# Kernel tuning notes

Measured on AMD Instinct MI355X. Metric: run time of the kernel, lower is better.

The kernel has to match this reference:

```python
import jax, jax.numpy as jnp
import numpy as np

B, H, S, D = 2, 8, 2048, 64
ALPHA = 1
P_NORM = 2
EPS = 1e-5


def setup_inputs() -> dict:
    key = jax.random.key(0)
    kq, kk, kv = jax.random.split(key, 3)
    query = jax.random.normal(kq, (B, H, S, D), dtype=jnp.float32)
    keys = jax.random.normal(kk, (B, H, S, D), dtype=jnp.float32)
    vals = jax.random.normal(kv, (B, H, S, D), dtype=jnp.float32)
    # causal mask: 1 where attention allowed, 0 elsewhere (masked_fill on mask==0)
    mask = jnp.tril(jnp.ones((S, S), dtype=jnp.int32))[None, None, :, :]
    return {"query": query, "keys": keys, "vals": vals, "mask": mask}


def reference(query, keys, vals, mask):
    d = query.shape[-1]
    sqrt_d = jnp.asarray(d, query.dtype) ** 0.5
    # L2-normalized cosine similarity term
    q_n = query / jnp.linalg.norm(query, axis=-1, keepdims=True)
    k_n = keys / jnp.linalg.norm(keys, axis=-1, keepdims=True)
    cos = jnp.einsum('bhqd,bhkd->bhqk', q_n, k_n)
    rq = (1.0 + (1.0 - cos) / (ALPHA * sqrt_d)) ** (-ALPHA)
    preattn = jnp.log(rq + EPS)
    # magnitude term: (||q||_p^p + ||k||_p^p) / (2 sqrt(d))
    q_mag = jnp.sum(jnp.abs(query) ** P_NORM, axis=-1, keepdims=True)  # [B,H,S,1]
    k_mag = jnp.sum(jnp.abs(keys) ** P_NORM, axis=-1, keepdims=True)   # [B,H,S,1]
    preattn = preattn + (q_mag + jnp.swapaxes(k_mag, -2, -1)) / (2.0 * sqrt_d)
    preattn = jnp.where(mask == 0, -jnp.inf, preattn)
    attn = jax.nn.softmax(preattn, axis=-1)
    out = jnp.einsum('bhqk,bhkd->bhqd', attn, vals)
    return out, attn
```

## Files before the change

kernel.cpp:

```cpp
#include <hip/hip_runtime.h>
#include <math.h>


#define BH 16
#define SS 2048
#define DD 64
#define NKT 32

typedef float f4a __attribute__((ext_vector_type(4)));
typedef short bs8 __attribute__((ext_vector_type(8)));
typedef short bs4 __attribute__((ext_vector_type(4)));

__device__ __forceinline__ short bf16rne(float f) {
  unsigned u = __float_as_uint(f);
  u += 0x7fffu + ((u >> 16) & 1u);
  return (short)(u >> 16);
}

__device__ __forceinline__ void bf16split(float f, short& hi, short& lo) {
  unsigned u = __float_as_uint(f);
  hi = (short)(u >> 16);
  float r = f - __uint_as_float(u & 0xffff0000u);
  lo = (short)(__float_as_uint(r) >> 16);
}

__global__ __launch_bounds__(256) void rq_rowss(const float* __restrict__ q,
                                                const float* __restrict__ k,
                                                float* __restrict__ ws) {
  int gid = blockIdx.x * 256 + threadIdx.x;
  int grp = gid >> 4;
  int lane = gid & 15;
  const int nrows = BH * SS;
  const float* src = (grp < nrows) ? q : k;
  int row = (grp < nrows) ? grp : (grp - nrows);
  float4 v = *(const float4*)(src + (size_t)row * DD + lane * 4);
  float s = v.x * v.x + v.y * v.y + v.z * v.z + v.w * v.w;
  s += __shfl_xor(s, 1);
  s += __shfl_xor(s, 2);
  s += __shfl_xor(s, 4);
  s += __shfl_xor(s, 8);
  if (lane == 0) ws[grp] = s;
}

__global__ __launch_bounds__(256) void rq_attn(const float* __restrict__ Q,
                                               const float* __restrict__ K,
                                               const float* __restrict__ V,
                                               const float* __restrict__ ss,
                                               float* __restrict__ outp,
                                               float* __restrict__ attnp) {
  __shared__ short Kf[4096];
  __shared__ short Vhi[4096];
  __shared__ short Vlo[4096];
  __shared__ float aLds[64 * 69];
  __shared__ float ektS[64];
  __shared__ float lrowp[2][64];
  __shared__ float lrow[64];

  const int t = threadIdx.x;
  const int bx = blockIdx.x;
  const int qt = NKT - 1 - (bx >> 4);
  const int bh = bx & 15;
  const int qbase = qt * 64;
  const float* Qg = Q + (size_t)bh * SS * DD;
  const float* Kg = K + (size_t)bh * SS * DD;
  const float* Vg = V + (size_t)bh * SS * DD;
  float* Ag = attnp + (size_t)bh * SS * SS;
  const float* qss = ss + (size_t)bh * SS;
  const float* kss = ss + (size_t)(BH * SS) + (size_t)bh * SS;

  const int l = t & 63;
  const int wv = t >> 6;
  const int qrh = wv >> 1;
  const int kch = wv & 1;
  const int l15 = l & 15;
  const int lh = (l >> 4) & 3;

  const int ukb = ((((l15 >> 2) & 3) | (((lh >> 1) & 1) << 2) | ((lh & 1) << 3) |
                    ((l15 & 3) << 4)) << 3);
  const int uvb = ((((l15 >> 2) & 3) | ((lh & 1) << 2) | ((l & 3) << 3) |
                    (((lh >> 1) & 1) << 7)) << 3);

  const int s_rb = (t >> 4) << 2;
  const int s_c0 = (t & 15) << 2;
  const int kw_ks = s_c0 >> 5;
  const int kw_dgrp = (s_c0 >> 3) & 3;
  const int kw_e0 = s_c0 & 7;
  const int kw_ub = (((t >> 4) & 3) | (((kw_dgrp >> 1) & 1) << 2) |
                     ((kw_dgrp & 1) << 3) | (((t >> 4) >> 2) << 6));
  const int vw_ks = s_rb >> 5;
  const int vw_kcgrp = (s_rb >> 3) & 3;
  const int vw_e0 = s_rb & 7;
  const int vw_ub = (((t & 15) & 3) | ((vw_kcgrp & 1) << 2) |
                     ((((t & 15) >> 2) & 3) << 5) | (((vw_kcgrp >> 1) & 1) << 7));

  auto stageK = [&](int kbase) {
#pragma unroll
    for (int i = 0; i < 4; ++i) {
      const int kc = s_rb + i;
      float4 v = *(const float4*)(Kg + (size_t)(kbase + kc) * DD + s_c0);
      float rn = rsqrtf(kss[kbase + kc]);
      bs4 b;
      b[0] = bf16rne(v.x * rn);
      b[1] = bf16rne(v.y * rn);
      b[2] = bf16rne(v.z * rn);
      b[3] = bf16rne(v.w * rn);
      *(bs4*)&Kf[kw_ks * 2048 + (kw_ub | (i << 4)) * 8 + kw_e0] = b;
    }
    if (t < 64) ektS[t] = __expf(kss[kbase + t] * 0.0625f);
  };

  bs8 qf[2][2];
#pragma unroll
  for (int mb = 0; mb < 2; ++mb) {
    const int row = qbase + qrh * 32 + mb * 16 + l15;
    const float rn = rsqrtf(qss[row]);
#pragma unroll
    for (int ks = 0; ks < 2; ++ks) {
      const float* src = Qg + (size_t)row * DD + ks * 32 + lh * 8;
      float4 x = *(const float4*)src;
      float4 y = *(const float4*)(src + 4);
      bs8 q;
      q[0] = bf16rne(x.x * rn);
      q[1] = bf16rne(x.y * rn);
      q[2] = bf16rne(x.z * rn);
      q[3] = bf16rne(x.w * rn);
      q[4] = bf16rne(y.x * rn);
      q[5] = bf16rne(y.y * rn);
      q[6] = bf16rne(y.z * rn);
      q[7] = bf16rne(y.w * rn);
      qf[mb][ks] = q;
    }
  }

  const f4a fz = {0.f, 0.f, 0.f, 0.f};

  float rs[8] = {0.f, 0.f, 0.f, 0.f, 0.f, 0.f, 0.f, 0.f};
  for (int kt = 0; kt <= qt; ++kt) {
    const int kbase = kt * 64;
    stageK(kbase);
    __syncthreads();

    f4a acc[4];
    acc[0] = fz; acc[1] = fz; acc[2] = fz; acc[3] = fz;
#pragma unroll
    for (int ks = 0; ks < 2; ++ks)
#pragma unroll
      for (int nb = 0; nb < 2; ++nb) {
        bs8 kf = *(const bs8*)&Kf[ks * 2048 + ((kch * 2 + nb) << 9) + ukb];
#pragma unroll
        for (int mb = 0; mb < 2; ++mb)
          acc[mb * 2 + nb] = __builtin_amdgcn_mfma_f32_16x16x32_bf16(
              qf[mb][ks], kf, acc[mb * 2 + nb], 0, 0, 0);
      }

    const float ek0 = ektS[kch * 32 + l15];
    const float ek1 = ektS[kch * 32 + 16 + l15];
    const bool diag = (kt == qt);
#pragma unroll
    for (int mb = 0; mb < 2; ++mb)
#pragma unroll
      for (int nb = 0; nb < 2; ++nb)
#pragma unroll
        for (int r = 0; r < 4; ++r) {
          float w = fmaf(8.0f, __builtin_amdgcn_rcpf(9.0f - acc[mb * 2 + nb][r]),
                         1e-5f) * (nb ? ek1 : ek0);
          const int col = kch * 32 + nb * 16 + l15;
          const int rowl = qrh * 32 + mb * 16 + lh * 4 + r;
          if (diag && col > rowl) w = 0.0f;
          rs[mb * 4 + r] += w;
        }
    __syncthreads();
  }

#pragma unroll
  for (int e = 0; e < 8; ++e) {
    float s = rs[e];
    s += __shfl_xor(s, 1);
    s += __shfl_xor(s, 2);
    s += __shfl_xor(s, 4);
    s += __shfl_xor(s, 8);
    rs[e] = s;
  }
  if (l15 == 0) {
#pragma unroll
    for (int mb = 0; mb < 2; ++mb)
#pragma unroll
      for (int r = 0; r < 4; ++r)
        lrowp[kch][qrh * 32 + mb * 16 + lh * 4 + r] = rs[mb * 4 + r];
  }
  __syncthreads();
  if (t < 64) lrow[t] = 1.0f / (lrowp[0][t] + lrowp[1][t]);
  __syncthreads();

  float li[8];
#pragma unroll
  for (int mb = 0; mb < 2; ++mb)
#pragma unroll
    for (int r = 0; r < 4; ++r)
      li[mb * 4 + r] = lrow[qrh * 32 + mb * 16 + lh * 4 + r];

  f4a O[4];
  O[0] = fz; O[1] = fz; O[2] = fz; O[3] = fz;
  for (int kt = 0; kt <= qt; ++kt) {
    const int kbase = kt * 64;
    stageK(kbase);
    {
      float mm[4][4];
#pragma unroll
      for (int i = 0; i < 4; ++i)
        *(float4*)&mm[i][0] =
            *(const float4*)(Vg + (size_t)(kbase + s_rb + i) * DD + s_c0);
#pragma unroll
      for (int j = 0; j < 4; ++j) {
        bs4 h4, l4;
#pragma unroll
        for (int i = 0; i < 4; ++i) {
          short hh, ll;
          bf16split(mm[i][j], hh, ll);
          h4[i] = hh;
          l4[i] = ll;
        }
        const int idx = vw_ks * 2048 + (vw_ub | (j << 3)) * 8 + vw_e0;
        *(bs4*)&Vhi[idx] = h4;
        *(bs4*)&Vlo[idx] = l4;
      }
    }
    __syncthreads();

    f4a acc[4];
    acc[0] = fz; acc[1] = fz; acc[2] = fz; acc[3] = fz;
#pragma unroll
    for (int ks = 0; ks < 2; ++ks)
#pragma unroll
      for (int nb = 0; nb < 2; ++nb) {
        bs8 kf = *(const bs8*)&Kf[ks * 2048 + ((kch * 2 + nb) << 9) + ukb];
#pragma unroll
        for (int mb = 0; mb < 2; ++mb)
          acc[mb * 2 + nb] = __builtin_amdgcn_mfma_f32_16x16x32_bf16(
              qf[mb][ks], kf, acc[mb * 2 + nb], 0, 0, 0);
      }

    {
      const float ek0 = ektS[kch * 32 + l15];
      const float ek1 = ektS[kch * 32 + 16 + l15];
      const bool diag = (kt == qt);
#pragma unroll
      for (int mb = 0; mb < 2; ++mb)
#pragma unroll
        for (int nb = 0; nb < 2; ++nb)
#pragma unroll
          for (int r = 0; r < 4; ++r) {
            float w = fmaf(8.0f,
                           __builtin_amdgcn_rcpf(9.0f - acc[mb * 2 + nb][r]),
                           1e-5f) * (nb ? ek1 : ek0);
            const int col = kch * 32 + nb * 16 + l15;
            const int rowl = qrh * 32 + mb * 16 + lh * 4 + r;
            if (diag && col > rowl) w = 0.0f;
            aLds[rowl * 69 + col] = w * li[mb * 4 + r];
          }
    }
    __syncthreads();

    {
      const int c0 = (t & 15) << 2;
      const int qr0 = t >> 4;
#pragma unroll
      for (int it = 0; it < 4; ++it) {
        const int qr = qr0 + it * 16;
        const float* ap = &aLds[qr * 69 + c0];
        *(float4*)(Ag + (size_t)(qbase + qr) * SS + kbase + c0) =
            make_float4(ap[0], ap[1], ap[2], ap[3]);
      }
    }

#pragma unroll
    for (int ks = 0; ks < 2; ++ks) {
      bs8 AH[2], AL[2];
#pragma unroll
      for (int mb = 0; mb < 2; ++mb) {
        const float* ap =
            &aLds[(qrh * 32 + mb * 16 + l15) * 69 + ks * 32 + lh * 8];
        bs8 hh, ll;
#pragma unroll
        for (int e = 0; e < 8; ++e) {
          short h, lo2;
          bf16split(ap[e], h, lo2);
          hh[e] = h;
          ll[e] = lo2;
        }
        AH[mb] = hh;
        AL[mb] = ll;
      }
#pragma unroll
      for (int nb = 0; nb < 2; ++nb) {
        const int vidx = ks * 2048 + ((kch * 2 + nb) << 8) + uvb;
        bs8 VH = *(const bs8*)&Vhi[vidx];
        bs8 VL = *(const bs8*)&Vlo[vidx];
#pragma unroll
        for (int mb = 0; mb < 2; ++mb) {
          O[mb * 2 + nb] = __builtin_amdgcn_mfma_f32_16x16x32_bf16(
              AH[mb], VH, O[mb * 2 + nb], 0, 0, 0);
          O[mb * 2 + nb] = __builtin_amdgcn_mfma_f32_16x16x32_bf16(
              AH[mb], VL, O[mb * 2 + nb], 0, 0, 0);
          O[mb * 2 + nb] = __builtin_amdgcn_mfma_f32_16x16x32_bf16(
              AL[mb], VH, O[mb * 2 + nb], 0, 0, 0);
        }
      }
    }
    __syncthreads();
  }

  {
    const float4 z = make_float4(0.f, 0.f, 0.f, 0.f);
    const int r0 = (t >> 4) << 2;
    const int c0 = (t & 15) << 2;
    for (int kt = qt + 1; kt < NKT; ++kt) {
#pragma unroll
      for (int i = 0; i < 4; ++i)
        *(float4*)(Ag + (size_t)(qbase + r0 + i) * SS + kt * 64 + c0) = z;
    }
  }

  {
    float* Og = outp + (size_t)bh * SS * DD;
#pragma unroll
    for (int mb = 0; mb < 2; ++mb)
#pragma unroll
      for (int nb = 0; nb < 2; ++nb)
#pragma unroll
        for (int r = 0; r < 4; ++r) {
          const int row = qbase + qrh * 32 + mb * 16 + lh * 4 + r;
          const int col = kch * 32 + nb * 16 + l15;
          Og[(size_t)row * DD + col] = O[mb * 2 + nb][r];
        }
  }
}

extern "C" void kernel_launch(void* const* d_in, const int* in_sizes, int n_in,
                              void* d_out, int out_size, void* d_ws, size_t ws_size,
                              hipStream_t stream) {
  const float* q = (const float*)d_in[0];
  const float* k = (const float*)d_in[1];
  const float* v = (const float*)d_in[2];
  float* out = (float*)d_out;
  float* attn = out + (size_t)BH * SS * DD;
  float* ws = (float*)d_ws;

  rq_rowss<<<dim3((2 * BH * SS) / 16), dim3(256), 0, stream>>>(q, k, ws);
  rq_attn<<<dim3(NKT * 16), dim3(256), 0, stream>>>(q, k, v, ws, out, attn);
}
```

Baseline: 386.6 us.

## Keep attention probabilities in registers by transposing QK^T MFMA and splitting PV over keys

Swaps the MFMA operands so the score accumulator comes out transposed, which lets each lane build the bf16 hi/lo A-fragments for the PV product directly in registers. This removes the aLds staging buffer and one barrier per tile. Attention-matrix writes become direct nontemporal float4 stores from registers, and V is stored transposed in an XOR-swizzled layout for 16x16x16 MFMAs. Each wave now accumulates over its half of the keys for all 64 dims, so a final LDS reduction across the two waves is needed. The row-sum reduction now uses fewer shuffles, and launch bounds request 3 blocks per CU.

```diff
diff --git a/kernel.cpp b/kernel.cpp
--- a/kernel.cpp
+++ b/kernel.cpp
@@ -10,18 +10,30 @@
 typedef float f4a __attribute__((ext_vector_type(4)));
 typedef short bs8 __attribute__((ext_vector_type(8)));
 typedef short bs4 __attribute__((ext_vector_type(4)));
+typedef unsigned int u32x2 __attribute__((ext_vector_type(2)));
 
 __device__ __forceinline__ short bf16rne(float f) {
   unsigned u = __float_as_uint(f);
   u += 0x7fffu + ((u >> 16) & 1u);
   return (short)(u >> 16);
 }
-
-__device__ __forceinline__ void bf16split(float f, short& hi, short& lo) {
-  unsigned u = __float_as_uint(f);
-  hi = (short)(u >> 16);
-  float r = f - __uint_as_float(u & 0xffff0000u);
-  lo = (short)(__float_as_uint(r) >> 16);
+__device__ __forceinline__ float truncb(float x) {
+  return __uint_as_float(__float_as_uint(x) & 0xffff0000u);
+}
+__device__ __forceinline__ unsigned packhi(float lo, float hi) {
+  return (__float_as_uint(hi) & 0xffff0000u) | (__float_as_uint(lo) >> 16);
+}
+
+__device__ __forceinline__ f4a mfma16(bs4 a, bs4 b, f4a c) {
+#if __has_builtin(__builtin_amdgcn_mfma_f32_16x16x16bf16_1k)
+  return __builtin_amdgcn_mfma_f32_16x16x16bf16_1k(a, b, c, 0, 0, 0);
+#else
+  f4a d;
+  asm("v_mfma_f32_16x16x16_bf16 %0, %1, %2, %3"
+      : "=v"(d)
+      : "v"(a), "v"(b), "v"(c));
+  return d;
+#endif
 }
 
 __global__ __launch_bounds__(256) void rq_rowss(const float* __restrict__ q,
@@ -42,19 +54,19 @@
   if (lane == 0) ws[grp] = s;
 }
 
-__global__ __launch_bounds__(256) void rq_attn(const float* __restrict__ Q,
-                                               const float* __restrict__ K,
-                                               const float* __restrict__ V,
-                                               const float* __restrict__ ss,
-                                               float* __restrict__ outp,
-                                               float* __restrict__ attnp) {
-  __shared__ short Kf[4096];
-  __shared__ short Vhi[4096];
-  __shared__ short Vlo[4096];
-  __shared__ float aLds[64 * 69];
+__global__ __launch_bounds__(256, 3) void rq_attn(const float* __restrict__ Q,
+                                                  const float* __restrict__ K,
+                                                  const float* __restrict__ V,
+                                                  const float* __restrict__ ss,
+                                                  float* __restrict__ outp,
+                                                  float* __restrict__ attnp) {
+  __shared__ short smemS[12288];
   __shared__ float ektS[64];
   __shared__ float lrowp[2][64];
   __shared__ float lrow[64];
+  short* const Kf = smemS;
+  short* const VtH = smemS + 4096;
+  short* const VtL = smemS + 8192;
 
   const int t = threadIdx.x;
   const int bx = blockIdx.x;
@@ -73,12 +85,10 @@
   const int qrh = wv >> 1;
   const int kch = wv & 1;
   const int l15 = l & 15;
-  const int lh = (l >> 4) & 3;
-
-  const int ukb = ((((l15 >> 2) & 3) | (((lh >> 1) & 1) << 2) | ((lh & 1) << 3) |
-                    ((l15 & 3) << 4)) << 3);
-  const int uvb = ((((l15 >> 2) & 3) | ((lh & 1) << 2) | ((l & 3) << 3) |
-                    (((lh >> 1) & 1) << 7)) << 3);
+  const int lh = l >> 4;
+
+  const int ukb = ((((l15 >> 2) & 3) | (((lh >> 1) & 1) << 2) |
+                    ((lh & 1) << 3) | ((l15 & 3) << 4)) << 3);
 
   const int s_rb = (t >> 4) << 2;
   const int s_c0 = (t & 15) << 2;
@@ -87,11 +97,6 @@
   const int kw_e0 = s_c0 & 7;
   const int kw_ub = (((t >> 4) & 3) | (((kw_dgrp >> 1) & 1) << 2) |
                      ((kw_dgrp & 1) << 3) | (((t >> 4) >> 2) << 6));
-  const int vw_ks = s_rb >> 5;
-  const int vw_kcgrp = (s_rb >> 3) & 3;
-  const int vw_e0 = s_rb & 7;
-  const int vw_ub = (((t & 15) & 3) | ((vw_kcgrp & 1) << 2) |
-                     ((((t & 15) >> 2) & 3) << 5) | (((vw_kcgrp >> 1) & 1) << 7));
 
   auto stageK = [&](int kbase) {
 #pragma unroll
@@ -107,6 +112,31 @@
       *(bs4*)&Kf[kw_ks * 2048 + (kw_ub | (i << 4)) * 8 + kw_e0] = b;
     }
     if (t < 64) ektS[t] = __expf(kss[kbase + t] * 0.0625f);
+  };
+
+  auto stageV = [&](int kbase) {
+    float mm[4][4];
+#pragma unroll
+    for (int i = 0; i < 4; ++i)
+      *(float4*)&mm[i][0] =
+          *(const float4*)(Vg + (size_t)(kbase + s_rb + i) * DD + s_c0);
+    const int kgw = t >> 4;
+#pragma unroll
+    for (int j = 0; j < 4; ++j) {
+      const int d = s_c0 + j;
+      const int si = (d * 16 + (kgw ^ (d & 15))) * 4;
+      u32x2 h, lo2;
+      h.x = packhi(mm[0][j], mm[1][j]);
+      h.y = packhi(mm[2][j], mm[3][j]);
+      float r0 = mm[0][j] - truncb(mm[0][j]);
+      float r1 = mm[1][j] - truncb(mm[1][j]);
+      float r2 = mm[2][j] - truncb(mm[2][j]);
+      float r3 = mm[3][j] - truncb(mm[3][j]);
+      lo2.x = packhi(r0, r1);
+      lo2.y = packhi(r2, r3);
+      *(u32x2*)&VtH[si] = h;
+      *(u32x2*)&VtL[si] = lo2;
+    }
   };
 
   bs8 qf[2][2];
@@ -134,7 +164,7 @@
 
   const f4a fz = {0.f, 0.f, 0.f, 0.f};
 
-  float rs[8] = {0.f, 0.f, 0.f, 0.f, 0.f, 0.f, 0.f, 0.f};
+  float rs0 = 0.f, rs1 = 0.f;
   for (int kt = 0; kt <= qt; ++kt) {
     const int kbase = kt * 64;
     stageK(kbase);
@@ -150,81 +180,55 @@
 #pragma unroll
         for (int mb = 0; mb < 2; ++mb)
           acc[mb * 2 + nb] = __builtin_amdgcn_mfma_f32_16x16x32_bf16(
-              qf[mb][ks], kf, acc[mb * 2 + nb], 0, 0, 0);
-      }
-
-    const float ek0 = ektS[kch * 32 + l15];
-    const float ek1 = ektS[kch * 32 + 16 + l15];
+              kf, qf[mb][ks], acc[mb * 2 + nb], 0, 0, 0);
+      }
+
     const bool diag = (kt == qt);
 #pragma unroll
-    for (int mb = 0; mb < 2; ++mb)
-#pragma unroll
-      for (int nb = 0; nb < 2; ++nb)
+    for (int nb = 0; nb < 2; ++nb) {
+      float ekr[4];
+#pragma unroll
+      for (int r = 0; r < 4; ++r)
+        ekr[r] = ektS[kch * 32 + nb * 16 + lh * 4 + r];
+#pragma unroll
+      for (int mb = 0; mb < 2; ++mb) {
+        const int qg = qrh * 32 + mb * 16 + l15;
 #pragma unroll
         for (int r = 0; r < 4; ++r) {
-          float w = fmaf(8.0f, __builtin_amdgcn_rcpf(9.0f - acc[mb * 2 + nb][r]),
-                         1e-5f) * (nb ? ek1 : ek0);
-          const int col = kch * 32 + nb * 16 + l15;
-          const int rowl = qrh * 32 + mb * 16 + lh * 4 + r;
-          if (diag && col > rowl) w = 0.0f;
-          rs[mb * 4 + r] += w;
+          const int kg = kch * 32 + nb * 16 + lh * 4 + r;
+          float w = fmaf(8.0f,
+                         __builtin_amdgcn_rcpf(9.0f - acc[mb * 2 + nb][r]),
+                         1e-5f) * ekr[r];
+          if (diag && kg > qg) w = 0.0f;
+          if (mb) rs1 += w; else rs0 += w;
         }
+      }
+    }
     __syncthreads();
   }
 
-#pragma unroll
-  for (int e = 0; e < 8; ++e) {
-    float s = rs[e];
-    s += __shfl_xor(s, 1);
-    s += __shfl_xor(s, 2);
-    s += __shfl_xor(s, 4);
-    s += __shfl_xor(s, 8);
-    rs[e] = s;
-  }
-  if (l15 == 0) {
-#pragma unroll
-    for (int mb = 0; mb < 2; ++mb)
-#pragma unroll
-      for (int r = 0; r < 4; ++r)
-        lrowp[kch][qrh * 32 + mb * 16 + lh * 4 + r] = rs[mb * 4 + r];
+  rs0 += __shfl_xor(rs0, 16);
+  rs0 += __shfl_xor(rs0, 32);
+  rs1 += __shfl_xor(rs1, 16);
+  rs1 += __shfl_xor(rs1, 32);
+  if (l < 16) {
+    lrowp[kch][qrh * 32 + l15] = rs0;
+    lrowp[kch][qrh * 32 + 16 + l15] = rs1;
   }
   __syncthreads();
   if (t < 64) lrow[t] = 1.0f / (lrowp[0][t] + lrowp[1][t]);
   __syncthreads();
-
-  float li[8];
-#pragma unroll
-  for (int mb = 0; mb < 2; ++mb)
-#pragma unroll
-    for (int r = 0; r < 4; ++r)
-      li[mb * 4 + r] = lrow[qrh * 32 + mb * 16 + lh * 4 + r];
-
-  f4a O[4];
-  O[0] = fz; O[1] = fz; O[2] = fz; O[3] = fz;
+  const float li0 = lrow[qrh * 32 + l15];
+  const float li1 = lrow[qrh * 32 + 16 + l15];
+
+  f4a O[8];
+#pragma unroll
+  for (int i = 0; i < 8; ++i) O[i] = fz;
+
   for (int kt = 0; kt <= qt; ++kt) {
     const int kbase = kt * 64;
     stageK(kbase);
-    {
-      float mm[4][4];
-#pragma unroll
-      for (int i = 0; i < 4; ++i)
-        *(float4*)&mm[i][0] =
-            *(const float4*)(Vg + (size_t)(kbase + s_rb + i) * DD + s_c0);
-#pragma unroll
-      for (int j = 0; j < 4; ++j) {
-        bs4 h4, l4;
-#pragma unroll
-        for (int i = 0; i < 4; ++i) {
-          short hh, ll;
-          bf16split(mm[i][j], hh, ll);
-          h4[i] = hh;
-          l4[i] = ll;
-        }
-        const int idx = vw_ks * 2048 + (vw_ub | (j << 3)) * 8 + vw_e0;
-        *(bs4*)&Vhi[idx] = h4;
-        *(bs4*)&Vlo[idx] = l4;
-      }
-    }
+    stageV(kbase);
     __syncthreads();
 
     f4a acc[4];
@@ -237,101 +241,103 @@
 #pragma unroll
         for (int mb = 0; mb < 2; ++mb)
           acc[mb * 2 + nb] = __builtin_amdgcn_mfma_f32_16x16x32_bf16(
-              qf[mb][ks], kf, acc[mb * 2 + nb], 0, 0, 0);
-      }
-
-    {
-      const float ek0 = ektS[kch * 32 + l15];
-      const float ek1 = ektS[kch * 32 + 16 + l15];
-      const bool diag = (kt == qt);
-#pragma unroll
-      for (int mb = 0; mb < 2; ++mb)
-#pragma unroll
-        for (int nb = 0; nb < 2; ++nb)
-#pragma unroll
-          for (int r = 0; r < 4; ++r) {
-            float w = fmaf(8.0f,
-                           __builtin_amdgcn_rcpf(9.0f - acc[mb * 2 + nb][r]),
-                           1e-5f) * (nb ? ek1 : ek0);
-            const int col = kch * 32 + nb * 16 + l15;
-            const int rowl = qrh * 32 + mb * 16 + lh * 4 + r;
-            if (diag && col > rowl) w = 0.0f;
-            aLds[rowl * 69 + col] = w * li[mb * 4 + r];
-          }
+              kf, qf[mb][ks], acc[mb * 2 + nb], 0, 0, 0);
+      }
+
+    u32x2 pH[2][2], pL[2][2];
+    const bool diag = (kt == qt);
+#pragma unroll
+    for (int nb = 0; nb < 2; ++nb) {
+      float ekr[4];
+#pragma unroll
+      for (int r = 0; r < 4; ++r)
+        ekr[r] = ektS[kch * 32 + nb * 16 + lh * 4 + r];
+#pragma unroll
+      for (int mb = 0; mb < 2; ++mb) {
+        const int qg = qrh * 32 + mb * 16 + l15;
+        const float li = mb ? li1 : li0;
+        float av[4];
+#pragma unroll
+        for (int r = 0; r < 4; ++r) {
+          const int kg = kch * 32 + nb * 16 + lh * 4 + r;
+          float w = fmaf(8.0f,
+                         __builtin_amdgcn_rcpf(9.0f - acc[mb * 2 + nb][r]),
+                         1e-5f) * ekr[r];
+          if (diag && kg > qg) w = 0.0f;
+          av[r] = w * li;
+        }
+        f4a a4 = {av[0], av[1], av[2], av[3]};
+        __builtin_nontemporal_store(
+            a4, (f4a*)(Ag + (size_t)(qbase + qg) * SS + kbase + kch * 32 +
+                       nb * 16 + lh * 4));
+        pH[mb][nb].x = packhi(av[0], av[1]);
+        pH[mb][nb].y = packhi(av[2], av[3]);
+        float r0 = av[0] - truncb(av[0]);
+        float r1 = av[1] - truncb(av[1]);
+        float r2 = av[2] - truncb(av[2]);
+        float r3 = av[3] - truncb(av[3]);
+        pL[mb][nb].x = packhi(r0, r1);
+        pL[mb][nb].y = packhi(r2, r3);
+      }
+    }
+
+#pragma unroll
+    for (int nb = 0; nb < 2; ++nb) {
+      const int kg = kch * 8 + nb * 4 + lh;
+#pragma unroll
+      for (int db = 0; db < 4; ++db) {
+        const int d = db * 16 + l15;
+        const int si = (d * 16 + (kg ^ (d & 15))) * 4;
+        bs4 VH = *(const bs4*)&VtH[si];
+        bs4 VL = *(const bs4*)&VtL[si];
+#pragma unroll
+        for (int mb = 0; mb < 2; ++mb) {
+          bs4 AH = __builtin_bit_cast(bs4, pH[mb][nb]);
+          bs4 AL = __builtin_bit_cast(bs4, pL[mb][nb]);
+          O[mb * 4 + db] = mfma16(AH, VH, O[mb * 4 + db]);
+          O[mb * 4 + db] = mfma16(AH, VL, O[mb * 4 + db]);
+          O[mb * 4 + db] = mfma16(AL, VH, O[mb * 4 + db]);
+        }
+      }
     }
     __syncthreads();
-
-    {
-      const int c0 = (t & 15) << 2;
-      const int qr0 = t >> 4;
-#pragma unroll
-      for (int it = 0; it < 4; ++it) {
-        const int qr = qr0 + it * 16;
-        const float* ap = &aLds[qr * 69 + c0];
-        *(float4*)(Ag + (size_t)(qbase + qr) * SS + kbase + c0) =
-            make_float4(ap[0], ap[1], ap[2], ap[3]);
-      }
-    }
-
-#pragma unroll
-    for (int ks = 0; ks < 2; ++ks) {
-      bs8 AH[2], AL[2];
-#pragma unroll
-      for (int mb = 0; mb < 2; ++mb) {
-        const float* ap =
-            &aLds[(qrh * 32 + mb * 16 + l15) * 69 + ks * 32 + lh * 8];
-        bs8 hh, ll;
-#pragma unroll
-        for (int e = 0; e < 8; ++e) {
-          short h, lo2;
-          bf16split(ap[e], h, lo2);
-          hh[e] = h;
-          ll[e] = lo2;
-        }
-        AH[mb] = hh;
-        AL[mb] = ll;
-      }
-#pragma unroll
-      for (int nb = 0; nb < 2; ++nb) {
-        const int vidx = ks * 2048 + ((kch * 2 + nb) << 8) + uvb;
-        bs8 VH = *(const bs8*)&Vhi[vidx];
-        bs8 VL = *(const bs8*)&Vlo[vidx];
-#pragma unroll
-        for (int mb = 0; mb < 2; ++mb) {
-          O[mb * 2 + nb] = __builtin_amdgcn_mfma_f32_16x16x32_bf16(
-              AH[mb], VH, O[mb * 2 + nb], 0, 0, 0);
-          O[mb * 2 + nb] = __builtin_amdgcn_mfma_f32_16x16x32_bf16(
-              AH[mb], VL, O[mb * 2 + nb], 0, 0, 0);
-          O[mb * 2 + nb] = __builtin_amdgcn_mfma_f32_16x16x32_bf16(
-              AL[mb], VH, O[mb * 2 + nb], 0, 0, 0);
-        }
-      }
-    }
-    __syncthreads();
   }
 
   {
-    const float4 z = make_float4(0.f, 0.f, 0.f, 0.f);
-    const int r0 = (t >> 4) << 2;
-    const int c0 = (t & 15) << 2;
+    const f4a z = {0.f, 0.f, 0.f, 0.f};
+    const int r0i = (t >> 4) << 2;
+    const int c0i = (t & 15) << 2;
     for (int kt = qt + 1; kt < NKT; ++kt) {
 #pragma unroll
       for (int i = 0; i < 4; ++i)
-        *(float4*)(Ag + (size_t)(qbase + r0 + i) * SS + kt * 64 + c0) = z;
-    }
-  }
-
-  {
+        __builtin_nontemporal_store(
+            z, (f4a*)(Ag + (size_t)(qbase + r0i + i) * SS + kt * 64 + c0i));
+    }
+  }
+
+  float* Osc = (float*)smemS;
+  if (kch == 1) {
+#pragma unroll
+    for (int mb = 0; mb < 2; ++mb)
+#pragma unroll
+      for (int db = 0; db < 4; ++db)
+#pragma unroll
+        for (int r = 0; r < 4; ++r)
+          Osc[(qrh * 32 + mb * 16 + lh * 4 + r) * 64 + db * 16 + l15] =
+              O[mb * 4 + db][r];
+  }
+  __syncthreads();
+  if (kch == 0) {
     float* Og = outp + (size_t)bh * SS * DD;
 #pragma unroll
     for (int mb = 0; mb < 2; ++mb)
 #pragma unroll
-      for (int nb = 0; nb < 2; ++nb)
+      for (int db = 0; db < 4; ++db)
 #pragma unroll
         for (int r = 0; r < 4; ++r) {
-          const int row = qbase + qrh * 32 + mb * 16 + lh * 4 + r;
-          const int col = kch * 32 + nb * 16 + l15;
-          Og[(size_t)row * DD + col] = O[mb * 2 + nb][r];
+          const int row = qrh * 32 + mb * 16 + lh * 4 + r;
+          Og[(size_t)(qbase + row) * DD + db * 16 + l15] =
+              O[mb * 4 + db][r] + Osc[row * 64 + db * 16 + l15];
         }
   }
 }
```

Result: slower. 399.1 us (+3.2%).
